# Performance work log

Hardware: AMD Instinct MI355X
Metric: run time of the kernel (lower is better)

The kernel has to match this reference:

```python
import jax, jax.numpy as jnp
import numpy as np

N_NODES = 100000
N_EDGES = 1600000
IN_CH, HID, OUT_CH = 500, 128, 40


def setup_inputs() -> dict:
    key = jax.random.key(0)
    ks = jax.random.split(key, 10)
    x = jax.random.normal(ks[0], (N_NODES, IN_CH), dtype=jnp.float32)
    edge_index = jax.random.randint(ks[1], (2, N_EDGES), 0, N_NODES, dtype=jnp.int64)
    edge_attr = jax.random.uniform(ks[2], (N_EDGES,), dtype=jnp.float32)
    def glorot(k, fan_in, fan_out):
        s = jnp.sqrt(6.0 / (fan_in + fan_out))
        return jax.random.uniform(k, (fan_in, fan_out), minval=-s, maxval=s, dtype=jnp.float32)
    return {
        "x": x, "edge_index": edge_index, "edge_attr": edge_attr,
        "W1": glorot(ks[3], IN_CH, HID), "b1": jnp.zeros((HID,), jnp.float32),
        "W2": glorot(ks[4], HID, HID), "b2": jnp.zeros((HID,), jnp.float32),
        "W3": glorot(ks[5], HID, OUT_CH), "b3": jnp.zeros((OUT_CH,), jnp.float32),
    }


def _gcn_norm(edge_index, edge_weight, num_nodes):
    # add self-loops with weight 1, then symmetric normalization D^-1/2 A D^-1/2
    loop = jnp.arange(num_nodes, dtype=edge_index.dtype)
    src = jnp.concatenate([edge_index[0], loop])
    dst = jnp.concatenate([edge_index[1], loop])
    ew = jnp.concatenate([edge_weight, jnp.ones((num_nodes,), edge_weight.dtype)])
    deg = jax.ops.segment_sum(ew, dst, num_segments=num_nodes)
    dinv = jnp.where(deg > 0, jax.lax.rsqrt(jnp.maximum(deg, 1e-12)), 0.0)
    norm = dinv[src] * ew * dinv[dst]
    return src, dst, norm


def _gcn_conv(x, W, b, src, dst, norm, num_nodes):
    h = x @ W                                   # [N, F_out] dense transform first
    msg = h[src] * norm[:, None]                # gather + scale  [E+N, F_out]
    out = jax.ops.segment_sum(msg, dst, num_segments=num_nodes)
    return out + b


def reference(x, edge_index, edge_attr, W1, b1, W2, b2, W3, b3):
    n = x.shape[0]
    src, dst, norm = _gcn_norm(edge_index, edge_attr, n)  # cached=False but graph is static
    # layer 1 (hidden) + relu + residual-dense (h_res starts at 0); dropout is identity in eval
    h = jax.nn.relu(_gcn_conv(x, W1, b1, src, dst, norm, n))
    h_res = h
    # layer 2 (hidden)
    h = jax.nn.relu(_gcn_conv(h, W2, b2, src, dst, norm, n)) + h_res
    # output layer
    out = _gcn_conv(h, W3, b3, src, dst, norm, n)
    return jax.nn.log_softmax(out, axis=-1)
```

## Files before the change

kernel.cpp:

```cpp
#include <hip/hip_runtime.h>
#include <hip/hip_bf16.h>
#include <type_traits>

#define NN 100000
#define NE 1600000

#define SCAN_E 1024
#define NBLK ((NN + SCAN_E - 1) / SCAN_E)
#define GBLK ((NN + 127) / 128)
#define EBLK ((NE + 511) / 512)
#define FBLK (NN / 16)

using f32x4 = __attribute__((ext_vector_type(4))) float;
using bf16x8 = __attribute__((ext_vector_type(8))) short;
using u16 = unsigned short;
using u32 = unsigned int;
using u64 = unsigned long long;

__device__ inline u16 f2bf(float f) {
    unsigned u = __float_as_uint(f);
    unsigned r = (u + 0x7fffu + ((u >> 16) & 1u)) >> 16;
    return (u16)r;
}
__device__ inline float bflo(unsigned u) { return __uint_as_float(u << 16); }
__device__ inline float bfhi(unsigned u) { return __uint_as_float(u & 0xffff0000u); }
__device__ inline float bf2f(u16 u) { return __uint_as_float((unsigned)u << 16); }
__device__ inline unsigned cvt2(float a, float b) {
    union { __hip_bfloat162 h; unsigned u; } c;
    c.h = __float22bfloat162_rn(make_float2(a, b));
    return c.u;
}

template <typename AT, int KLIM, int KSTEPS, bool TAIL>
__device__ __forceinline__ void gemm_body(const AT* __restrict__ X,
                                          const short* __restrict__ Wp,
                                          u16* __restrict__ Out, int gblk) {
    const int lane = threadIdx.x & 63;
    const int wave = threadIdx.x >> 6;
    const int row0 = gblk * 128 + wave * 16;
    const int arow = row0 + (lane & 15);
    const int kgrp = (lane >> 4) << 3;
    const bool rvalid = arow < NN;
    const AT* aptr = X + (size_t)arow * KLIM + kgrp;
    const bf16x8* wp = reinterpret_cast<const bf16x8*>(Wp);

    f32x4 acc[8];
#pragma unroll
    for (int nt = 0; nt < 8; nt++) acc[nt] = (f32x4){0.f, 0.f, 0.f, 0.f};

    const int FULL = TAIL ? (KSTEPS - 1) : KSTEPS;
#pragma unroll 2
    for (int ks = 0; ks < FULL; ks++) {
        bf16x8 af;
        if (rvalid) {
            if constexpr (std::is_same_v<AT, float>) {
                f32x4 f0 = __builtin_nontemporal_load(
                    reinterpret_cast<const f32x4*>(aptr + ks * 32));
                f32x4 f1 = __builtin_nontemporal_load(
                    reinterpret_cast<const f32x4*>(aptr + ks * 32 + 4));
                union { bf16x8 v; unsigned u[4]; } a;
                a.u[0] = cvt2(f0.x, f0.y);
                a.u[1] = cvt2(f0.z, f0.w);
                a.u[2] = cvt2(f1.x, f1.y);
                a.u[3] = cvt2(f1.z, f1.w);
                af = a.v;
            } else {
                af = *reinterpret_cast<const bf16x8*>(aptr + ks * 32);
            }
        } else {
#pragma unroll
            for (int j = 0; j < 8; j++) af[j] = 0;
        }
#pragma unroll
        for (int nt = 0; nt < 8; nt++) {
            bf16x8 bf = wp[(ks * 8 + nt) * 64 + lane];
            acc[nt] = __builtin_amdgcn_mfma_f32_16x16x32_bf16(af, bf, acc[nt], 0, 0, 0);
        }
    }
    if (TAIL) {
        const int ks = KSTEPS - 1;
        bf16x8 af;
#pragma unroll
        for (int j = 0; j < 8; j++) {
            int k = ks * 32 + kgrp + j;
            bool ok = rvalid && k < KLIM;
            if constexpr (std::is_same_v<AT, float>) {
                af[j] = (short)f2bf(ok ? aptr[ks * 32 + j] : 0.f);
            } else {
                af[j] = ok ? (short)aptr[ks * 32 + j] : (short)0;
            }
        }
#pragma unroll
        for (int nt = 0; nt < 8; nt++) {
            bf16x8 bf = wp[(ks * 8 + nt) * 64 + lane];
            acc[nt] = __builtin_amdgcn_mfma_f32_16x16x32_bf16(af, bf, acc[nt], 0, 0, 0);
        }
    }

    const int rbase = row0 + ((lane >> 4) << 2);
    const int cbase = lane & 15;
#pragma unroll
    for (int r = 0; r < 4; r++) {
        int orow = rbase + r;
        if (orow < NN) {
            u16* p = Out + (size_t)orow * 128 + cbase;
#pragma unroll
            for (int nt = 0; nt < 8; nt += 2) {
                unsigned v = cvt2(acc[nt][r], acc[nt + 1][r]);
                p[nt * 16] = (u16)v;
                p[nt * 16 + 16] = (u16)(v >> 16);
            }
        }
    }
}

__global__ __launch_bounds__(512) void k_gemm1_deg(const float* __restrict__ X,
                                                   const short* __restrict__ Wp,
                                                   u16* __restrict__ Out,
                                                   const int* __restrict__ ei,
                                                   const float* __restrict__ ea,
                                                   u32* __restrict__ dc,
                                                   int* __restrict__ rank) {
    if (blockIdx.x >= GBLK) {
        int e = (blockIdx.x - GBLK) * 512 + threadIdx.x;
        if (e < NE) {
            int d = ei[NE + e];
            u32 add = (1u << 24) | (u32)(ea[e] * 32768.0f);
            u32 old = atomicAdd(dc + d, add);
            rank[e] = (int)(old >> 24);
        }
        return;
    }
    gemm_body<float, 500, 16, true>(X, Wp, Out, blockIdx.x);
}

__global__ __launch_bounds__(256) void k_scatter(const int* __restrict__ ei,
                                                 const float* __restrict__ ea,
                                                 const float* __restrict__ dinv,
                                                 const int* __restrict__ row_ptr,
                                                 const int* __restrict__ rank,
                                                 int2* __restrict__ csr) {
    int e = blockIdx.x * 256 + threadIdx.x;
    if (e >= NE) return;
    int s = ei[e], d = ei[NE + e];
    int pos = row_ptr[d] + rank[e];
    float w = dinv[s] * ea[e] * dinv[d];
    csr[pos] = make_int2(s, __float_as_int(w));
}

__global__ __launch_bounds__(256) void k_scan1(const u32* __restrict__ dc,
                                               int* __restrict__ row_ptr,
                                               int* __restrict__ part,
                                               float* __restrict__ dinv) {
    __shared__ int ts[256];
    const int tid = threadIdx.x;
    int base = blockIdx.x * SCAN_E + tid * 4;
    int v[4];
    int ssum = 0;
#pragma unroll
    for (int j = 0; j < 4; j++) {
        if (base + j < NN) {
            u32 d2 = dc[base + j];
            v[j] = (int)(d2 >> 24);
            dinv[base + j] = rsqrtf((float)(d2 & 0xFFFFFFu) * (1.0f / 32768.0f) + 1.0f);
        } else {
            v[j] = 0;
        }
        ssum += v[j];
    }
    ts[tid] = ssum;
    __syncthreads();
    for (int o = 1; o < 256; o <<= 1) {
        int t = (tid >= o) ? ts[tid - o] : 0;
        __syncthreads();
        ts[tid] += t;
        __syncthreads();
    }
    int excl = ts[tid] - ssum;
#pragma unroll
    for (int j = 0; j < 4; j++) {
        if (base + j < NN) row_ptr[base + j] = excl;
        excl += v[j];
    }
    if (tid == 255) part[blockIdx.x] = ts[255];
}

__global__ void k_scan2(int* __restrict__ part) {
    if (threadIdx.x == 0) {
        int acc = 0;
        for (int b = 0; b < NBLK; b++) { int t = part[b]; part[b] = acc; acc += t; }
    }
}

__global__ __launch_bounds__(256) void k_scan3(int* __restrict__ row_ptr,
                                               const int* __restrict__ part) {
    int base = blockIdx.x * SCAN_E + threadIdx.x * 4;
    int off = part[blockIdx.x];
#pragma unroll
    for (int j = 0; j < 4; j++)
        if (base + j < NN) row_ptr[base + j] += off;
    if (blockIdx.x == 0 && threadIdx.x == 0) row_ptr[NN] = NE;
}

__global__ __launch_bounds__(256) void k_packW(const float* __restrict__ W,
                                               short* __restrict__ Wp,
                                               int K, int total) {
    int t = blockIdx.x * 256 + threadIdx.x;
    if (t >= total) return;
    int lane = t & 63;
    int nt = (t >> 6) & 7;
    int ks = t >> 9;
    int col = nt * 16 + (lane & 15);
    int kb = ks * 32 + ((lane >> 4) << 3);
    bf16x8 v;
#pragma unroll
    for (int j = 0; j < 8; j++) {
        int k = kb + j;
        v[j] = (k < K) ? (short)f2bf(W[(size_t)k * 128 + col]) : (short)0;
    }
    reinterpret_cast<bf16x8*>(Wp)[t] = v;
}

__global__ __launch_bounds__(256) void k_packW3(const float* __restrict__ W,
                                                short* __restrict__ Wp) {
    int t = blockIdx.x * 256 + threadIdx.x;
    if (t >= 768) return;
    int lane = t & 63;
    int nt = (t >> 6) % 3;
    int ks = t / 192;
    int col = nt * 16 + (lane & 15);
    int kb = ks * 32 + ((lane >> 4) << 3);
    bf16x8 v;
#pragma unroll
    for (int j = 0; j < 8; j++)
        v[j] = (col < 40) ? (short)f2bf(W[(size_t)(kb + j) * 40 + col]) : (short)0;
    reinterpret_cast<bf16x8*>(Wp)[t] = v;
}

template <int MODE>
__global__ __launch_bounds__(512) void k_pull_fused(const u16* __restrict__ H,
                                                    const int* __restrict__ row_ptr,
                                                    const int2* __restrict__ csr,
                                                    const float* __restrict__ dinv,
                                                    const float* __restrict__ b,
                                                    const u16* __restrict__ R,
                                                    u16* __restrict__ OutRow,
                                                    const short* __restrict__ Wg,
                                                    u16* __restrict__ OutG) {
    __shared__ u16 tile[16][136];
    const int nl = threadIdx.x >> 5;
    const int node = blockIdx.x * 16 + nl;
    const int cg = threadIdx.x & 31;
    const uint2* H2v = reinterpret_cast<const uint2*>(H);

    float dv = dinv[node];
    float sw = dv * dv;
    uint2 h = H2v[node * 32 + cg];
    float4 acc;
    acc.x = bflo(h.x) * sw; acc.y = bfhi(h.x) * sw;
    acc.z = bflo(h.y) * sw; acc.w = bfhi(h.y) * sw;

    int e0 = row_ptr[node], e1 = row_ptr[node + 1];
    for (int base = e0; base < e1; base += 32) {
        int n = e1 - base;
        if (n > 32) n = 32;
        int2 sv = (cg < n) ? csr[base + cg] : make_int2(0, 0);
        int j = 0;
        for (; j + 4 <= n; j += 4) {
            int s0 = __shfl(sv.x, j + 0, 32);
            int s1 = __shfl(sv.x, j + 1, 32);
            int s2 = __shfl(sv.x, j + 2, 32);
            int s3 = __shfl(sv.x, j + 3, 32);
            float w0 = __int_as_float(__shfl(sv.y, j + 0, 32));
            float w1 = __int_as_float(__shfl(sv.y, j + 1, 32));
            float w2 = __int_as_float(__shfl(sv.y, j + 2, 32));
            float w3 = __int_as_float(__shfl(sv.y, j + 3, 32));
            uint2 g0 = H2v[s0 * 32 + cg];
            uint2 g1 = H2v[s1 * 32 + cg];
            uint2 g2 = H2v[s2 * 32 + cg];
            uint2 g3 = H2v[s3 * 32 + cg];
            acc.x = fmaf(w0, bflo(g0.x), acc.x); acc.y = fmaf(w0, bfhi(g0.x), acc.y);
            acc.z = fmaf(w0, bflo(g0.y), acc.z); acc.w = fmaf(w0, bfhi(g0.y), acc.w);
            acc.x = fmaf(w1, bflo(g1.x), acc.x); acc.y = fmaf(w1, bfhi(g1.x), acc.y);
            acc.z = fmaf(w1, bflo(g1.y), acc.z); acc.w = fmaf(w1, bfhi(g1.y), acc.w);
            acc.x = fmaf(w2, bflo(g2.x), acc.x); acc.y = fmaf(w2, bfhi(g2.x), acc.y);
            acc.z = fmaf(w2, bflo(g2.y), acc.z); acc.w = fmaf(w2, bfhi(g2.y), acc.w);
            acc.x = fmaf(w3, bflo(g3.x), acc.x); acc.y = fmaf(w3, bfhi(g3.x), acc.y);
            acc.z = fmaf(w3, bflo(g3.y), acc.z); acc.w = fmaf(w3, bfhi(g3.y), acc.w);
        }
        for (; j < n; j++) {
            int s = __shfl(sv.x, j, 32);
            float w = __int_as_float(__shfl(sv.y, j, 32));
            uint2 g = H2v[s * 32 + cg];
            acc.x = fmaf(w, bflo(g.x), acc.x); acc.y = fmaf(w, bfhi(g.x), acc.y);
            acc.z = fmaf(w, bflo(g.y), acc.z); acc.w = fmaf(w, bfhi(g.y), acc.w);
        }
    }

    float4 bb = reinterpret_cast<const float4*>(b)[cg];
    float4 o;
    o.x = fmaxf(acc.x + bb.x, 0.f);
    o.y = fmaxf(acc.y + bb.y, 0.f);
    o.z = fmaxf(acc.z + bb.z, 0.f);
    o.w = fmaxf(acc.w + bb.w, 0.f);
    if (MODE == 2) {
        uint2 r = reinterpret_cast<const uint2*>(R)[node * 32 + cg];
        o.x += bflo(r.x); o.y += bfhi(r.x);
        o.z += bflo(r.y); o.w += bfhi(r.y);
    }
    uint2 pk = make_uint2(cvt2(o.x, o.y), cvt2(o.z, o.w));
    *reinterpret_cast<uint2*>(&tile[nl][cg * 4]) = pk;
    if (MODE == 1)
        reinterpret_cast<uint2*>(OutRow)[node * 32 + cg] = pk;

    __syncthreads();

    const int lane = threadIdx.x & 63;
    const int wave = threadIdx.x >> 6;
    const int NT = (MODE == 1) ? 8 : 3;
    if (wave < NT) {
        const bf16x8* wp = reinterpret_cast<const bf16x8*>(Wg);
        f32x4 gacc = (f32x4){0.f, 0.f, 0.f, 0.f};
        const int arow = lane & 15;
        const int kg = (lane >> 4) << 3;
#pragma unroll
        for (int ks = 0; ks < 4; ks++) {
            bf16x8 af = *reinterpret_cast<const bf16x8*>(&tile[arow][ks * 32 + kg]);
            bf16x8 bf = wp[(ks * NT + wave) * 64 + lane];
            gacc = __builtin_amdgcn_mfma_f32_16x16x32_bf16(af, bf, gacc, 0, 0, 0);
        }
        const int rb = ((lane >> 4) << 2);
        const int cb = lane & 15;
        if (MODE == 1) {
            u16* p = OutG + (size_t)(blockIdx.x * 16 + rb) * 128 + wave * 16 + cb;
#pragma unroll
            for (int r = 0; r < 4; r++) p[(size_t)r * 128] = f2bf(gacc[r]);
        } else {
            int col = wave * 16 + cb;
            if (col < 40) {
                u16* p = OutG + (size_t)(blockIdx.x * 16 + rb) * 64 + col;
#pragma unroll
                for (int r = 0; r < 4; r++) p[(size_t)r * 64] = f2bf(gacc[r]);
            }
        }
    }
}

__global__ __launch_bounds__(256) void k_pull40_lsm(const u16* __restrict__ G,
                                                    const int* __restrict__ row_ptr,
                                                    const int2* __restrict__ csr,
                                                    const float* __restrict__ dinv,
                                                    const float* __restrict__ b3,
                                                    float* __restrict__ out) {
    int node = blockIdx.x * 4 + (threadIdx.x >> 6);
    int lane = threadIdx.x & 63;
    const bool act = lane < 40;
    float dv = dinv[node];
    float sw = dv * dv;
    float acc = act ? bf2f(G[node * 64 + lane]) * sw : 0.f;

    int e0 = row_ptr[node], e1 = row_ptr[node + 1];
    for (int base = e0; base < e1; base += 64) {
        int n = e1 - base;
        if (n > 64) n = 64;
        int2 sv = (lane < n) ? csr[base + lane] : make_int2(0, 0);
        int j = 0;
        for (; j + 4 <= n; j += 4) {
            int s0 = __shfl(sv.x, j + 0);
            int s1 = __shfl(sv.x, j + 1);
            int s2 = __shfl(sv.x, j + 2);
            int s3 = __shfl(sv.x, j + 3);
            float w0 = __int_as_float(__shfl(sv.y, j + 0));
            float w1 = __int_as_float(__shfl(sv.y, j + 1));
            float w2 = __int_as_float(__shfl(sv.y, j + 2));
            float w3 = __int_as_float(__shfl(sv.y, j + 3));
            float g0 = act ? bf2f(G[s0 * 64 + lane]) : 0.f;
            float g1 = act ? bf2f(G[s1 * 64 + lane]) : 0.f;
            float g2 = act ? bf2f(G[s2 * 64 + lane]) : 0.f;
            float g3 = act ? bf2f(G[s3 * 64 + lane]) : 0.f;
            acc = fmaf(w0, g0, acc);
            acc = fmaf(w1, g1, acc);
            acc = fmaf(w2, g2, acc);
            acc = fmaf(w3, g3, acc);
        }
        for (; j < n; j++) {
            int s = __shfl(sv.x, j);
            float w = __int_as_float(__shfl(sv.y, j));
            float g = act ? bf2f(G[s * 64 + lane]) : 0.f;
            acc = fmaf(w, g, acc);
        }
    }

    float v = act ? acc + b3[lane] : -1e30f;
    float m = v;
    for (int o = 32; o; o >>= 1) m = fmaxf(m, __shfl_xor(m, o));
    float e = act ? expf(v - m) : 0.f;
    float ssum = e;
    for (int o = 32; o; o >>= 1) ssum += __shfl_xor(ssum, o);
    float ls = logf(ssum);
    if (act) out[node * 40 + lane] = v - m - ls;
}

extern "C" void kernel_launch(void* const* d_in, const int* in_sizes, int n_in,
                              void* d_out, int out_size, void* d_ws, size_t ws_size,
                              hipStream_t stream) {
    const float* x  = (const float*)d_in[0];
    const int*   ei = (const int*)d_in[1];
    const float* ea = (const float*)d_in[2];
    const float* W1 = (const float*)d_in[3];
    const float* b1 = (const float*)d_in[4];
    const float* W2 = (const float*)d_in[5];
    const float* b2 = (const float*)d_in[6];
    const float* W3 = (const float*)d_in[7];
    const float* b3 = (const float*)d_in[8];
    float* out = (float*)d_out;

    short* Wp1     = (short*)d_ws;
    short* Wp2     = Wp1 + 65536;
    short* Wp3     = Wp2 + 16384;
    u16*   Hb      = (u16*)(Wp3 + 6144);
    u16*   h1b     = Hb + (size_t)NN * 128;
    u16*   H2      = h1b + (size_t)NN * 128;
    u16*   G3b     = H2 + (size_t)NN * 128;
    u32*   dc      = (u32*)(G3b + (size_t)NN * 64);
    float* dinv    = (float*)(dc + NN);
    int*   row_ptr = (int*)(dinv + NN);
    int*   part    = row_ptr + NN + 8;
    int*   rank    = part + 128;
    int2*  csr     = (int2*)(rank + NE);

    hipMemsetAsync(dc, 0, NN * sizeof(u32), stream);
    k_packW<<<32, 256, 0, stream>>>(W1, Wp1, 500, 16 * 8 * 64);
    k_packW<<<8, 256, 0, stream>>>(W2, Wp2, 128, 4 * 8 * 64);
    k_packW3<<<3, 256, 0, stream>>>(W3, Wp3);

    k_gemm1_deg<<<GBLK + EBLK, 512, 0, stream>>>(x, Wp1, Hb, ei, ea, dc, rank);

    k_scan1<<<NBLK, 256, 0, stream>>>(dc, row_ptr, part, dinv);
    k_scan2<<<1, 64, 0, stream>>>(part);
    k_scan3<<<NBLK, 256, 0, stream>>>(row_ptr, part);

    k_scatter<<<(NE + 255) / 256, 256, 0, stream>>>(ei, ea, dinv, row_ptr, rank, csr);

    k_pull_fused<1><<<FBLK, 512, 0, stream>>>(Hb, row_ptr, csr, dinv, b1, nullptr,
                                              h1b, Wp2, H2);

    k_pull_fused<2><<<FBLK, 512, 0, stream>>>(H2, row_ptr, csr, dinv, b2, h1b,
                                              nullptr, Wp3, G3b);

    k_pull40_lsm<<<NN / 4, 256, 0, stream>>>(G3b, row_ptr, csr, dinv, b3, out);
}
```

Before: 453.7 us.

## Replace global degree atomics with LDS-partitioned per-chunk histograms

Degree counting and per-edge rank assignment move from global atomics on a degree array into shared-memory histograms. Each of 256 blocks owns one of 8 destination partitions and one of 32 edge chunks, and writes its counts per chunk. The scan then builds per-chunk prefix offsets that the scatter adds to compute CSR positions. This removes global atomic contention and the memset, at the cost of extra count and prefix arrays (32×NN entries each), and every histogram block reads its whole edge chunk again for each partition. The three weight-pack kernels are also merged into one launch.

```diff
diff --git a/kernel.cpp b/kernel.cpp
--- a/kernel.cpp
+++ b/kernel.cpp
@@ -8,8 +8,11 @@
 #define SCAN_E 1024
 #define NBLK ((NN + SCAN_E - 1) / SCAN_E)
 #define GBLK ((NN + 127) / 128)
-#define EBLK ((NE + 511) / 512)
 #define FBLK (NN / 16)
+#define PSZ 12500
+#define CSZ 50000
+#define NCH 32
+#define HBLK 256
 
 using f32x4 = __attribute__((ext_vector_type(4))) float;
 using bf16x8 = __attribute__((ext_vector_type(8))) short;
@@ -114,41 +117,42 @@
     }
 }
 
-__global__ __launch_bounds__(512) void k_gemm1_deg(const float* __restrict__ X,
-                                                   const short* __restrict__ Wp,
-                                                   u16* __restrict__ Out,
-                                                   const int* __restrict__ ei,
-                                                   const float* __restrict__ ea,
-                                                   u32* __restrict__ dc,
-                                                   int* __restrict__ rank) {
-    if (blockIdx.x >= GBLK) {
-        int e = (blockIdx.x - GBLK) * 512 + threadIdx.x;
-        if (e < NE) {
+__global__ __launch_bounds__(512) void k_hist_gemm1(const float* __restrict__ X,
+                                                    const short* __restrict__ Wp,
+                                                    u16* __restrict__ Out,
+                                                    const int* __restrict__ ei,
+                                                    const float* __restrict__ ea,
+                                                    u32* __restrict__ counts,
+                                                    int* __restrict__ rank) {
+    __shared__ u32 hist[PSZ];
+    if (blockIdx.x < HBLK) {
+        const int p = blockIdx.x >> 5;
+        const int c = blockIdx.x & 31;
+        const int dbase = p * PSZ;
+        for (int i = threadIdx.x; i < PSZ; i += 512) hist[i] = 0;
+        __syncthreads();
+        const int ebeg = c * CSZ;
+#pragma unroll 2
+        for (int e = ebeg + (int)threadIdx.x; e < ebeg + CSZ; e += 512) {
             int d = ei[NE + e];
-            u32 add = (1u << 24) | (u32)(ea[e] * 32768.0f);
-            u32 old = atomicAdd(dc + d, add);
-            rank[e] = (int)(old >> 24);
-        }
+            float w = ea[e];
+            unsigned rel = (unsigned)(d - dbase);
+            if (rel < PSZ) {
+                u32 add = (1u << 24) | (u32)(w * 32768.0f);
+                u32 old = atomicAdd(&hist[rel], add);
+                rank[e] = (int)(old >> 24);
+            }
+        }
+        __syncthreads();
+        for (int i = threadIdx.x; i < PSZ; i += 512)
+            counts[(size_t)c * NN + dbase + i] = hist[i];
         return;
     }
-    gemm_body<float, 500, 16, true>(X, Wp, Out, blockIdx.x);
-}
-
-__global__ __launch_bounds__(256) void k_scatter(const int* __restrict__ ei,
-                                                 const float* __restrict__ ea,
-                                                 const float* __restrict__ dinv,
-                                                 const int* __restrict__ row_ptr,
-                                                 const int* __restrict__ rank,
-                                                 int2* __restrict__ csr) {
-    int e = blockIdx.x * 256 + threadIdx.x;
-    if (e >= NE) return;
-    int s = ei[e], d = ei[NE + e];
-    int pos = row_ptr[d] + rank[e];
-    float w = dinv[s] * ea[e] * dinv[d];
-    csr[pos] = make_int2(s, __float_as_int(w));
-}
-
-__global__ __launch_bounds__(256) void k_scan1(const u32* __restrict__ dc,
+    gemm_body<float, 500, 16, true>(X, Wp, Out, blockIdx.x - HBLK);
+}
+
+__global__ __launch_bounds__(256) void k_scan1(const u32* __restrict__ counts,
+                                               u16* __restrict__ cpfx,
                                                int* __restrict__ row_ptr,
                                                int* __restrict__ part,
                                                float* __restrict__ dinv) {
@@ -159,10 +163,16 @@
     int ssum = 0;
 #pragma unroll
     for (int j = 0; j < 4; j++) {
-        if (base + j < NN) {
-            u32 d2 = dc[base + j];
-            v[j] = (int)(d2 >> 24);
-            dinv[base + j] = rsqrtf((float)(d2 & 0xFFFFFFu) * (1.0f / 32768.0f) + 1.0f);
+        int d = base + j;
+        if (d < NN) {
+            u32 acc = 0;
+#pragma unroll
+            for (int c = 0; c < NCH; c++) {
+                cpfx[(size_t)c * NN + d] = (u16)(acc >> 24);
+                acc += counts[(size_t)c * NN + d];
+            }
+            v[j] = (int)(acc >> 24);
+            dinv[d] = rsqrtf((float)(acc & 0xFFFFFFu) * (1.0f / 32768.0f) + 1.0f);
         } else {
             v[j] = 0;
         }
@@ -202,11 +212,24 @@
     if (blockIdx.x == 0 && threadIdx.x == 0) row_ptr[NN] = NE;
 }
 
-__global__ __launch_bounds__(256) void k_packW(const float* __restrict__ W,
-                                               short* __restrict__ Wp,
-                                               int K, int total) {
-    int t = blockIdx.x * 256 + threadIdx.x;
-    if (t >= total) return;
+__global__ __launch_bounds__(256) void k_scatter(const int* __restrict__ ei,
+                                                 const float* __restrict__ ea,
+                                                 const float* __restrict__ dinv,
+                                                 const int* __restrict__ row_ptr,
+                                                 const u16* __restrict__ cpfx,
+                                                 const int* __restrict__ rank,
+                                                 int2* __restrict__ csr) {
+    int e = blockIdx.x * 256 + threadIdx.x;
+    if (e >= NE) return;
+    int s = ei[e], d = ei[NE + e];
+    int c = e / CSZ;
+    int pos = row_ptr[d] + (int)cpfx[(size_t)c * NN + d] + rank[e];
+    float w = dinv[s] * ea[e] * dinv[d];
+    csr[pos] = make_int2(s, __float_as_int(w));
+}
+
+__device__ __forceinline__ void pack128(const float* __restrict__ W,
+                                        short* __restrict__ Wp, int K, int t) {
     int lane = t & 63;
     int nt = (t >> 6) & 7;
     int ks = t >> 9;
@@ -221,20 +244,30 @@
     reinterpret_cast<bf16x8*>(Wp)[t] = v;
 }
 
-__global__ __launch_bounds__(256) void k_packW3(const float* __restrict__ W,
-                                                short* __restrict__ Wp) {
+__global__ __launch_bounds__(256) void k_packAll(const float* __restrict__ W1,
+                                                 const float* __restrict__ W2,
+                                                 const float* __restrict__ W3,
+                                                 short* __restrict__ Wp1,
+                                                 short* __restrict__ Wp2,
+                                                 short* __restrict__ Wp3) {
     int t = blockIdx.x * 256 + threadIdx.x;
-    if (t >= 768) return;
-    int lane = t & 63;
-    int nt = (t >> 6) % 3;
-    int ks = t / 192;
-    int col = nt * 16 + (lane & 15);
-    int kb = ks * 32 + ((lane >> 4) << 3);
-    bf16x8 v;
-#pragma unroll
-    for (int j = 0; j < 8; j++)
-        v[j] = (col < 40) ? (short)f2bf(W[(size_t)(kb + j) * 40 + col]) : (short)0;
-    reinterpret_cast<bf16x8*>(Wp)[t] = v;
+    if (t < 8192) {
+        pack128(W1, Wp1, 500, t);
+    } else if (t < 10240) {
+        pack128(W2, Wp2, 128, t - 8192);
+    } else if (t < 11008) {
+        int tt = t - 10240;
+        int lane = tt & 63;
+        int nt = (tt >> 6) % 3;
+        int ks = tt / 192;
+        int col = nt * 16 + (lane & 15);
+        int kb = ks * 32 + ((lane >> 4) << 3);
+        bf16x8 v;
+#pragma unroll
+        for (int j = 0; j < 8; j++)
+            v[j] = (col < 40) ? (short)f2bf(W3[(size_t)(kb + j) * 40 + col]) : (short)0;
+        reinterpret_cast<bf16x8*>(Wp3)[tt] = v;
+    }
 }
 
 template <int MODE>
@@ -420,27 +453,26 @@
     short* Wp3     = Wp2 + 16384;
     u16*   Hb      = (u16*)(Wp3 + 6144);
     u16*   h1b     = Hb + (size_t)NN * 128;
-    u16*   H2      = h1b + (size_t)NN * 128;
+    u16*   H2     = h1b + (size_t)NN * 128;
     u16*   G3b     = H2 + (size_t)NN * 128;
-    u32*   dc      = (u32*)(G3b + (size_t)NN * 64);
-    float* dinv    = (float*)(dc + NN);
+    float* dinv    = (float*)(G3b + (size_t)NN * 64);
     int*   row_ptr = (int*)(dinv + NN);
     int*   part    = row_ptr + NN + 8;
     int*   rank    = part + 128;
-    int2*  csr     = (int2*)(rank + NE);
-
-    hipMemsetAsync(dc, 0, NN * sizeof(u32), stream);
-    k_packW<<<32, 256, 0, stream>>>(W1, Wp1, 500, 16 * 8 * 64);
-    k_packW<<<8, 256, 0, stream>>>(W2, Wp2, 128, 4 * 8 * 64);
-    k_packW3<<<3, 256, 0, stream>>>(W3, Wp3);
-
-    k_gemm1_deg<<<GBLK + EBLK, 512, 0, stream>>>(x, Wp1, Hb, ei, ea, dc, rank);
-
-    k_scan1<<<NBLK, 256, 0, stream>>>(dc, row_ptr, part, dinv);
+    u32*   counts  = (u32*)(rank + NE);
+    u16*   cpfx    = (u16*)(counts + (size_t)NCH * NN);
+    int2*  csr     = (int2*)(cpfx + (size_t)NCH * NN);
+
+    k_packAll<<<43, 256, 0, stream>>>(W1, W2, W3, Wp1, Wp2, Wp3);
+
+    k_hist_gemm1<<<HBLK + GBLK, 512, 0, stream>>>(x, Wp1, Hb, ei, ea, counts, rank);
+
+    k_scan1<<<NBLK, 256, 0, stream>>>(counts, cpfx, row_ptr, part, dinv);
     k_scan2<<<1, 64, 0, stream>>>(part);
     k_scan3<<<NBLK, 256, 0, stream>>>(row_ptr, part);
 
-    k_scatter<<<(NE + 255) / 256, 256, 0, stream>>>(ei, ea, dinv, row_ptr, rank, csr);
+    k_scatter<<<(NE + 255) / 256, 256, 0, stream>>>(ei, ea, dinv, row_ptr, cpfx,
+                                                    rank, csr);
 
     k_pull_fused<1><<<FBLK, 512, 0, stream>>>(Hb, row_ptr, csr, dinv, b1, nullptr,
                                               h1b, Wp2, H2);
```

Measured after the change: 436.7 us. 3.7% less time.
